# Kernel optimization log

Hardware: AMD Instinct MI355X
Metric: run time of the kernel (lower is better)

The kernel has to match this reference:

```python
import jax, jax.numpy as jnp
import numpy as np

N_NODES = 100000
D_FEAT = 128
N_EDGES = 1500000
H1 = 2 * D_FEAT  # 256, input to first linear (concat of src/dst feats)
H2 = 128


def setup_inputs() -> dict:
    key = jax.random.key(0)
    k_x, k_e, k_w1, k_w2 = jax.random.split(key, 4)
    x = jax.random.normal(k_x, (N_NODES, D_FEAT), dtype=jnp.float32)
    edge_label_index = jax.random.randint(k_e, (2, N_EDGES), 0, N_NODES, dtype=jnp.int64)
    # Kaiming-ish small init for stability
    W1 = jax.random.normal(k_w1, (H1, H2), dtype=jnp.float32) * (1.0 / np.sqrt(H1))
    b1 = jnp.zeros((H2,), dtype=jnp.float32)
    W2 = jax.random.normal(k_w2, (H2, 1), dtype=jnp.float32) * (1.0 / np.sqrt(H2))
    b2 = jnp.zeros((1,), dtype=jnp.float32)
    return {"x": x, "edge_label_index": edge_label_index,
            "W1": W1, "b1": b1, "W2": W2, "b2": b2}


def reference(x, edge_label_index, W1, b1, W2, b2):
    row, col = edge_label_index[0], edge_label_index[1]
    # gather node pair features and concat: [E, 2*D]
    h = jnp.concatenate([x[row], x[col]], axis=-1)
    h = jax.nn.relu(h @ W1 + b1)  # [E, H2]
    out = h @ W2 + b2             # [E, 1]
    return out.reshape(-1)        # [E]
```

## Files before the change

### kernel.cpp

```cpp
#include <hip/hip_runtime.h>
#include <hip/hip_bf16.h>
#include <stdint.h>

typedef __attribute__((ext_vector_type(8))) short s16x8;
typedef __attribute__((ext_vector_type(8))) unsigned short u16x8;
typedef __attribute__((ext_vector_type(4))) float f32x4;

#define D_FEAT 128
#define H2 128
#define BLOCK_THREADS 512
#define WAVES 8
#define MW 32
#define EPB (WAVES * MW)

__device__ __forceinline__ unsigned short f2bf(float f) {
  uint32_t u = __float_as_uint(f);
  return (unsigned short)((u + 0x7fffu + ((u >> 16) & 1u)) >> 16);
}

__global__ void k_cvt_x(const float* __restrict__ x, unsigned short* __restrict__ xb, int n8) {
  int i = blockIdx.x * blockDim.x + threadIdx.x;
  if (i >= n8) return;
  const f32x4* p = (const f32x4*)x + (size_t)i * 2;
  f32x4 a = p[0], b = p[1];
  u16x8 o;
  o[0] = f2bf(a[0]); o[1] = f2bf(a[1]); o[2] = f2bf(a[2]); o[3] = f2bf(a[3]);
  o[4] = f2bf(b[0]); o[5] = f2bf(b[1]); o[6] = f2bf(b[2]); o[7] = f2bf(b[3]);
  ((u16x8*)xb)[i] = o;
}

__global__ void k_cvt_w1(const float* __restrict__ W1, unsigned short* __restrict__ w1s) {
  int tid = blockIdx.x * blockDim.x + threadIdx.x;
  int lane = tid & 63;
  int kkf  = tid >> 6;
  int kk = kkf >> 3, f = kkf & 7;
  int c = lane & 15, g = lane >> 4;
  int n = f * 16 + c;
  u16x8 o;
#pragma unroll
  for (int j = 0; j < 8; ++j)
    o[j] = f2bf(W1[(kk * 32 + g * 8 + j) * H2 + n]);
  ((u16x8*)w1s)[tid] = o;
}

template <bool XBF>
__global__ __launch_bounds__(BLOCK_THREADS, 4)
void k_edge_mlp(const float* __restrict__ xf,
                const unsigned short* __restrict__ xb,
                const int* __restrict__ eli,
                const float* __restrict__ W1,
                const unsigned short* __restrict__ w1ws,
                const float* __restrict__ b1,
                const float* __restrict__ W2,
                const float* __restrict__ b2,
                float* __restrict__ out, int E, int nNodes)
{
  __shared__ alignas(16) unsigned short w1t[H2 * 256];
  const int t0   = threadIdx.x;
  const int lane = t0 & 63;
  const int wid  = t0 >> 6;
  const int c    = lane & 15;
  const int g    = lane >> 4;

  if (XBF) {
#pragma unroll
    for (int i = 0; i < 8; ++i) {
      int idx = i * BLOCK_THREADS + t0;
      ((u16x8*)w1t)[idx] = ((const u16x8*)w1ws)[idx];
    }
  } else {
#pragma unroll
    for (int i = 0; i < 8; ++i) {
      int chunk = i * BLOCK_THREADS + t0;
      int cl  = chunk & 63;
      int kkf = chunk >> 6;
      int kk = kkf >> 3, f = kkf & 7;
      int cc = cl & 15, gg = cl >> 4;
      int n = f * 16 + cc;
      u16x8 o;
#pragma unroll
      for (int j = 0; j < 8; ++j)
        o[j] = f2bf(W1[(kk * 32 + gg * 8 + j) * H2 + n]);
      ((u16x8*)w1t)[chunk] = o;
    }
  }

  const int gbase = blockIdx.x * EPB + wid * MW;
  unsigned ro[2], co[2];
#pragma unroll
  for (int m = 0; m < 2; ++m) {
    int e = gbase + m * 16 + c;
    e = e < E ? e : E - 1;
    int nr = eli[e];
    int nc = eli[E + e];
    nr = nr < 0 ? 0 : (nr >= nNodes ? nNodes - 1 : nr);
    nc = nc < 0 ? 0 : (nc >= nNodes ? nNodes - 1 : nc);
    ro[m] = (unsigned)nr * D_FEAT + g * 8;
    co[m] = (unsigned)nc * D_FEAT + g * 8;
  }

  __syncthreads();

  auto loadA = [&](int kk, s16x8* dst) {
#pragma unroll
    for (int m = 0; m < 2; ++m) {
      unsigned off = (kk < 4 ? ro[m] : co[m]) + (unsigned)((kk & 3) * 32);
      if (XBF) {
        dst[m] = *(const s16x8*)(xb + off);
      } else {
        const f32x4* q = (const f32x4*)(xf + off);
        f32x4 a = q[0], b = q[1];
        s16x8 v;
        v[0] = (short)f2bf(a[0]); v[1] = (short)f2bf(a[1]);
        v[2] = (short)f2bf(a[2]); v[3] = (short)f2bf(a[3]);
        v[4] = (short)f2bf(b[0]); v[5] = (short)f2bf(b[1]);
        v[6] = (short)f2bf(b[2]); v[7] = (short)f2bf(b[3]);
        dst[m] = v;
      }
    }
  };

  f32x4 acc[2][8];
#pragma unroll
  for (int m = 0; m < 2; ++m)
#pragma unroll
    for (int f = 0; f < 8; ++f) {
      f32x4 z = {0.f, 0.f, 0.f, 0.f};
      acc[m][f] = z;
    }

  s16x8 abuf[2][2];
  loadA(0, abuf[0]);
  loadA(1, abuf[1]);

  const unsigned short* bbase = w1t + (unsigned)lane * 8;

#pragma unroll
  for (int kk = 0; kk < 8; ++kk) {
    __builtin_amdgcn_s_setprio(1);
#pragma unroll
    for (int f = 0; f < 8; ++f) {
      s16x8 bfrag = *(const s16x8*)(bbase + (kk * 8 + f) * 512);
#pragma unroll
      for (int m = 0; m < 2; ++m)
        acc[m][f] = __builtin_amdgcn_mfma_f32_16x16x32_bf16(abuf[kk & 1][m], bfrag, acc[m][f], 0, 0, 0);
    }
    __builtin_amdgcn_s_setprio(0);
    if (kk < 6) loadA(kk + 2, abuf[kk & 1]);
  }

  float b1v[8], w2v[8];
#pragma unroll
  for (int f = 0; f < 8; ++f) {
    b1v[f] = b1[f * 16 + c];
    w2v[f] = W2[f * 16 + c];
  }
  const float b2s = b2[0];

#pragma unroll
  for (int m = 0; m < 2; ++m) {
    float sr[4];
#pragma unroll
    for (int r = 0; r < 4; ++r) {
      float s = 0.f;
#pragma unroll
      for (int f = 0; f < 8; ++f) {
        float h = acc[m][f][r] + b1v[f];
        h = h > 0.f ? h : 0.f;
        s += h * w2v[f];
      }
#pragma unroll
      for (int msk = 1; msk < 16; msk <<= 1)
        s += __shfl_xor(s, msk, 64);
      sr[r] = s;
    }
    int ebase = gbase + m * 16 + g * 4;
    if (c == 0 && ebase < E) {
      f32x4 o = {sr[0] + b2s, sr[1] + b2s, sr[2] + b2s, sr[3] + b2s};
      *(f32x4*)(out + ebase) = o;
    }
  }
}

extern "C" void kernel_launch(void* const* d_in, const int* in_sizes, int n_in,
                              void* d_out, int out_size, void* d_ws, size_t ws_size,
                              hipStream_t stream) {
  const float* x   = (const float*)d_in[0];
  const int*   eli = (const int*)d_in[1];
  const float* W1  = (const float*)d_in[2];
  const float* b1  = (const float*)d_in[3];
  const float* W2  = (const float*)d_in[4];
  const float* b2  = (const float*)d_in[5];
  float* out = (float*)d_out;

  const int E      = in_sizes[1] / 2;
  const int nNodes = in_sizes[0] / D_FEAT;

  const size_t xbytes = (size_t)nNodes * D_FEAT * 2;
  const size_t need   = xbytes + 65536;
  const bool bfpath   = (ws_size >= need);

  const int grid = (E + EPB - 1) / EPB;

  if (bfpath) {
    unsigned short* xbw  = (unsigned short*)d_ws;
    unsigned short* w1sw = (unsigned short*)((char*)d_ws + xbytes);
    int n8 = nNodes * D_FEAT / 8;
    k_cvt_x<<<(n8 + 255) / 256, 256, 0, stream>>>(x, xbw, n8);
    k_cvt_w1<<<16, 256, 0, stream>>>(W1, w1sw);
    k_edge_mlp<true><<<grid, BLOCK_THREADS, 0, stream>>>(
        x, xbw, eli, W1, w1sw, b1, W2, b2, out, E, nNodes);
  } else {
    k_edge_mlp<false><<<grid, BLOCK_THREADS, 0, stream>>>(
        x, nullptr, eli, W1, nullptr, b1, W2, b2, out, E, nNodes);
  }
}
```

Measured before the change: 137.2 us.

## Process several edge tiles per block and prefetch next tile's gathers

Each block now loops over four edge tiles instead of one, so the 64 KB W1 shared-memory staging is amortized across more work. While the epilogue (bias, ReLU, W2 dot and shuffle reduction) runs for the current tile, the next tile's indices and first A fragments are already loaded. This cuts the number of blocks by four, which reduces parallelism and may leave CUs idle at the tail.

Result: slower. 197.8 us (+44.1%).

```diff
diff --git a/kernel.cpp b/kernel.cpp
--- a/kernel.cpp
+++ b/kernel.cpp
@@ -12,6 +12,7 @@
 #define WAVES 8
 #define MW 32
 #define EPB (WAVES * MW)
+#define TPB 4
 
 __device__ __forceinline__ unsigned short f2bf(float f) {
   uint32_t u = __float_as_uint(f);
@@ -85,23 +86,26 @@
     }
   }
 
-  const int gbase = blockIdx.x * EPB + wid * MW;
-  unsigned ro[2], co[2];
-#pragma unroll
-  for (int m = 0; m < 2; ++m) {
-    int e = gbase + m * 16 + c;
-    e = e < E ? e : E - 1;
-    int nr = eli[e];
-    int nc = eli[E + e];
-    nr = nr < 0 ? 0 : (nr >= nNodes ? nNodes - 1 : nr);
-    nc = nc < 0 ? 0 : (nc >= nNodes ? nNodes - 1 : nc);
-    ro[m] = (unsigned)nr * D_FEAT + g * 8;
-    co[m] = (unsigned)nc * D_FEAT + g * 8;
-  }
-
-  __syncthreads();
-
-  auto loadA = [&](int kk, s16x8* dst) {
+  const int nt = (E + EPB - 1) / EPB;
+  int tile = blockIdx.x * TPB;
+  if (tile >= nt) return;
+  const int tend = (tile + TPB < nt) ? tile + TPB : nt;
+
+  auto mkoff = [&](int tt, unsigned* ro, unsigned* co) {
+#pragma unroll
+    for (int m = 0; m < 2; ++m) {
+      int e = tt * EPB + wid * MW + m * 16 + c;
+      e = e < E ? e : E - 1;
+      int nr = eli[e];
+      int nc = eli[E + e];
+      nr = nr < 0 ? 0 : (nr >= nNodes ? nNodes - 1 : nr);
+      nc = nc < 0 ? 0 : (nc >= nNodes ? nNodes - 1 : nc);
+      ro[m] = (unsigned)nr * D_FEAT + g * 8;
+      co[m] = (unsigned)nc * D_FEAT + g * 8;
+    }
+  };
+
+  auto loadA = [&](const unsigned* ro, const unsigned* co, int kk, s16x8* dst) {
 #pragma unroll
     for (int m = 0; m < 2; ++m) {
       unsigned off = (kk < 4 ? ro[m] : co[m]) + (unsigned)((kk & 3) * 32);
@@ -120,65 +124,92 @@
     }
   };
 
-  f32x4 acc[2][8];
-#pragma unroll
-  for (int m = 0; m < 2; ++m)
+  __syncthreads();
+
+  const unsigned short* bbase = w1t + (unsigned)lane * 8;
+
+  unsigned ro[2], co[2];
+  mkoff(tile, ro, co);
+  s16x8 abuf[2][2];
+  loadA(ro, co, 0, abuf[0]);
+  loadA(ro, co, 1, abuf[1]);
+
+  const float b2s = b2[0];
+
+  while (true) {
+    f32x4 acc[2][8];
+#pragma unroll
+    for (int m = 0; m < 2; ++m)
+#pragma unroll
+      for (int f = 0; f < 8; ++f) {
+        f32x4 z = {0.f, 0.f, 0.f, 0.f};
+        acc[m][f] = z;
+      }
+
+#pragma unroll
+    for (int kk = 0; kk < 8; ++kk) {
+      __builtin_amdgcn_s_setprio(1);
+#pragma unroll
+      for (int f = 0; f < 8; ++f) {
+        s16x8 bfrag = *(const s16x8*)(bbase + (kk * 8 + f) * 512);
+#pragma unroll
+        for (int m = 0; m < 2; ++m)
+          acc[m][f] = __builtin_amdgcn_mfma_f32_16x16x32_bf16(abuf[kk & 1][m], bfrag, acc[m][f], 0, 0, 0);
+      }
+      __builtin_amdgcn_s_setprio(0);
+      if (kk < 6) loadA(ro, co, kk + 2, abuf[kk & 1]);
+    }
+
+    float b1v[8], w2v[8];
 #pragma unroll
     for (int f = 0; f < 8; ++f) {
-      f32x4 z = {0.f, 0.f, 0.f, 0.f};
-      acc[m][f] = z;
-    }
-
-  s16x8 abuf[2][2];
-  loadA(0, abuf[0]);
-  loadA(1, abuf[1]);
-
-  const unsigned short* bbase = w1t + (unsigned)lane * 8;
-
-#pragma unroll
-  for (int kk = 0; kk < 8; ++kk) {
-    __builtin_amdgcn_s_setprio(1);
-#pragma unroll
-    for (int f = 0; f < 8; ++f) {
-      s16x8 bfrag = *(const s16x8*)(bbase + (kk * 8 + f) * 512);
-#pragma unroll
-      for (int m = 0; m < 2; ++m)
-        acc[m][f] = __builtin_amdgcn_mfma_f32_16x16x32_bf16(abuf[kk & 1][m], bfrag, acc[m][f], 0, 0, 0);
-    }
-    __builtin_amdgcn_s_setprio(0);
-    if (kk < 6) loadA(kk + 2, abuf[kk & 1]);
-  }
-
-  float b1v[8], w2v[8];
-#pragma unroll
-  for (int f = 0; f < 8; ++f) {
-    b1v[f] = b1[f * 16 + c];
-    w2v[f] = W2[f * 16 + c];
-  }
-  const float b2s = b2[0];
-
-#pragma unroll
-  for (int m = 0; m < 2; ++m) {
-    float sr[4];
-#pragma unroll
-    for (int r = 0; r < 4; ++r) {
-      float s = 0.f;
-#pragma unroll
-      for (int f = 0; f < 8; ++f) {
-        float h = acc[m][f][r] + b1v[f];
-        h = h > 0.f ? h : 0.f;
-        s += h * w2v[f];
-      }
-#pragma unroll
-      for (int msk = 1; msk < 16; msk <<= 1)
-        s += __shfl_xor(s, msk, 64);
-      sr[r] = s;
-    }
-    int ebase = gbase + m * 16 + g * 4;
-    if (c == 0 && ebase < E) {
-      f32x4 o = {sr[0] + b2s, sr[1] + b2s, sr[2] + b2s, sr[3] + b2s};
-      *(f32x4*)(out + ebase) = o;
-    }
+      b1v[f] = b1[f * 16 + c];
+      w2v[f] = W2[f * 16 + c];
+    }
+    float pre[2][4];
+#pragma unroll
+    for (int m = 0; m < 2; ++m)
+#pragma unroll
+      for (int r = 0; r < 4; ++r) {
+        float s = 0.f;
+#pragma unroll
+        for (int f = 0; f < 8; ++f) {
+          float h = acc[m][f][r] + b1v[f];
+          h = h > 0.f ? h : 0.f;
+          s += h * w2v[f];
+        }
+        pre[m][r] = s;
+      }
+
+    const int gbase = tile * EPB + wid * MW;
+    const bool more = (tile + 1 < tend);
+
+    if (more) {
+      mkoff(tile + 1, ro, co);
+      loadA(ro, co, 0, abuf[0]);
+      loadA(ro, co, 1, abuf[1]);
+    }
+
+#pragma unroll
+    for (int m = 0; m < 2; ++m) {
+      float sr[4];
+#pragma unroll
+      for (int r = 0; r < 4; ++r) {
+        float s = pre[m][r];
+#pragma unroll
+        for (int msk = 1; msk < 16; msk <<= 1)
+          s += __shfl_xor(s, msk, 64);
+        sr[r] = s;
+      }
+      int ebase = gbase + m * 16 + g * 4;
+      if (c == 0 && ebase < E) {
+        f32x4 o = {sr[0] + b2s, sr[1] + b2s, sr[2] + b2s, sr[3] + b2s};
+        *(f32x4*)(out + ebase) = o;
+      }
+    }
+
+    if (!more) break;
+    ++tile;
   }
 }
 
@@ -200,7 +231,8 @@
   const size_t need   = xbytes + 65536;
   const bool bfpath   = (ws_size >= need);
 
-  const int grid = (E + EPB - 1) / EPB;
+  const int nt   = (E + EPB - 1) / EPB;
+  const int grid = (nt + TPB - 1) / TPB;
 
   if (bfpath) {
     unsigned short* xbw  = (unsigned short*)d_ws;
```

## Precompute per-node W1 projections and reduce edge MLP to gather-add-dot

Applied to the files above, without the earlier changes.

Uses linearity of the first layer to split [x_r, x_c] @ W1 into per-node projections u = x@W1_top + b1 and v = x@W1_bot, computed once per node with MFMA and stored as bf16. The edge kernel then only gathers u[row] and v[col], applies ReLU to the sum and takes the dot product with W2. This removes the per-edge matmul, which is about 15x more work than the per-node one, at the cost of an extra pass writing two node-sized tables. It also adds a second bf16 rounding of the intermediate projections.

After: 148.2 us. +8.0%, slower.

```diff
diff --git a/kernel.cpp b/kernel.cpp
--- a/kernel.cpp
+++ b/kernel.cpp
@@ -8,25 +8,13 @@
 
 #define D_FEAT 128
 #define H2 128
-#define BLOCK_THREADS 512
-#define WAVES 8
-#define MW 32
-#define EPB (WAVES * MW)
 
 __device__ __forceinline__ unsigned short f2bf(float f) {
   uint32_t u = __float_as_uint(f);
   return (unsigned short)((u + 0x7fffu + ((u >> 16) & 1u)) >> 16);
 }
-
-__global__ void k_cvt_x(const float* __restrict__ x, unsigned short* __restrict__ xb, int n8) {
-  int i = blockIdx.x * blockDim.x + threadIdx.x;
-  if (i >= n8) return;
-  const f32x4* p = (const f32x4*)x + (size_t)i * 2;
-  f32x4 a = p[0], b = p[1];
-  u16x8 o;
-  o[0] = f2bf(a[0]); o[1] = f2bf(a[1]); o[2] = f2bf(a[2]); o[3] = f2bf(a[3]);
-  o[4] = f2bf(b[0]); o[5] = f2bf(b[1]); o[6] = f2bf(b[2]); o[7] = f2bf(b[3]);
-  ((u16x8*)xb)[i] = o;
+__device__ __forceinline__ float bf2f(unsigned short s) {
+  return __uint_as_float((uint32_t)s << 16);
 }
 
 __global__ void k_cvt_w1(const float* __restrict__ W1, unsigned short* __restrict__ w1s) {
@@ -43,80 +31,217 @@
   ((u16x8*)w1s)[tid] = o;
 }
 
-template <bool XBF>
-__global__ __launch_bounds__(BLOCK_THREADS, 4)
-void k_edge_mlp(const float* __restrict__ xf,
-                const unsigned short* __restrict__ xb,
+__global__ void k_cvt_w2p(const float* __restrict__ W2, float* __restrict__ w2p) {
+  int s = threadIdx.x;
+  w2p[s] = W2[(s & 7) * 16 + (s >> 3)];
+}
+
+__global__ __launch_bounds__(256, 4)
+void k_uv(const float* __restrict__ x,
+          const unsigned short* __restrict__ w1ws,
+          const float* __restrict__ b1,
+          unsigned short* __restrict__ u,
+          unsigned short* __restrict__ v,
+          int nNodes)
+{
+  __shared__ alignas(16) unsigned short w1t[H2 * 256];
+  const int t0 = threadIdx.x, lane = t0 & 63, wid = t0 >> 6;
+  const int c = lane & 15, g = lane >> 4;
+
+#pragma unroll
+  for (int i = 0; i < 16; ++i) {
+    int idx = i * 256 + t0;
+    ((u16x8*)w1t)[idx] = ((const u16x8*)w1ws)[idx];
+  }
+
+  const int nb = blockIdx.x * 128 + wid * 32;
+  s16x8 af[4][2];
+#pragma unroll
+  for (int m = 0; m < 2; ++m) {
+    int node = nb + m * 16 + c;
+    node = node < nNodes ? node : nNodes - 1;
+    const float* xp = x + (size_t)node * D_FEAT;
+#pragma unroll
+    for (int kk = 0; kk < 4; ++kk) {
+      const f32x4* q = (const f32x4*)(xp + kk * 32 + g * 8);
+      f32x4 a = q[0], b = q[1];
+      s16x8 vv;
+      vv[0] = (short)f2bf(a[0]); vv[1] = (short)f2bf(a[1]);
+      vv[2] = (short)f2bf(a[2]); vv[3] = (short)f2bf(a[3]);
+      vv[4] = (short)f2bf(b[0]); vv[5] = (short)f2bf(b[1]);
+      vv[6] = (short)f2bf(b[2]); vv[7] = (short)f2bf(b[3]);
+      af[kk][m] = vv;
+    }
+  }
+  float b1v[8];
+#pragma unroll
+  for (int f = 0; f < 8; ++f) b1v[f] = b1[f * 16 + c];
+
+  __syncthreads();
+  const unsigned short* bbase = w1t + (unsigned)lane * 8;
+
+  f32x4 acc[2][8];
+
+#pragma unroll
+  for (int m = 0; m < 2; ++m)
+#pragma unroll
+    for (int f = 0; f < 8; ++f) {
+      f32x4 z = {b1v[f], b1v[f], b1v[f], b1v[f]};
+      acc[m][f] = z;
+    }
+#pragma unroll
+  for (int kk = 0; kk < 4; ++kk)
+#pragma unroll
+    for (int f = 0; f < 8; ++f) {
+      s16x8 bfrag = *(const s16x8*)(bbase + (kk * 8 + f) * 512);
+#pragma unroll
+      for (int m = 0; m < 2; ++m)
+        acc[m][f] = __builtin_amdgcn_mfma_f32_16x16x32_bf16(af[kk][m], bfrag, acc[m][f], 0, 0, 0);
+    }
+#pragma unroll
+  for (int m = 0; m < 2; ++m)
+#pragma unroll
+    for (int r = 0; r < 4; ++r) {
+      int node = nb + m * 16 + g * 4 + r;
+      if (node < nNodes) {
+        u16x8 o;
+#pragma unroll
+        for (int f = 0; f < 8; ++f) o[f] = f2bf(acc[m][f][r]);
+        *(u16x8*)(u + (size_t)node * H2 + c * 8) = o;
+      }
+    }
+
+#pragma unroll
+  for (int m = 0; m < 2; ++m)
+#pragma unroll
+    for (int f = 0; f < 8; ++f) {
+      f32x4 z = {0.f, 0.f, 0.f, 0.f};
+      acc[m][f] = z;
+    }
+#pragma unroll
+  for (int kk = 0; kk < 4; ++kk)
+#pragma unroll
+    for (int f = 0; f < 8; ++f) {
+      s16x8 bfrag = *(const s16x8*)(bbase + ((kk + 4) * 8 + f) * 512);
+#pragma unroll
+      for (int m = 0; m < 2; ++m)
+        acc[m][f] = __builtin_amdgcn_mfma_f32_16x16x32_bf16(af[kk][m], bfrag, acc[m][f], 0, 0, 0);
+    }
+#pragma unroll
+  for (int m = 0; m < 2; ++m)
+#pragma unroll
+    for (int r = 0; r < 4; ++r) {
+      int node = nb + m * 16 + g * 4 + r;
+      if (node < nNodes) {
+        u16x8 o;
+#pragma unroll
+        for (int f = 0; f < 8; ++f) o[f] = f2bf(acc[m][f][r]);
+        *(u16x8*)(v + (size_t)node * H2 + c * 8) = o;
+      }
+    }
+}
+
+__global__ __launch_bounds__(256, 8)
+void k_edge(const unsigned short* __restrict__ u,
+            const unsigned short* __restrict__ v,
+            const int* __restrict__ eli,
+            const float* __restrict__ w2p,
+            const float* __restrict__ b2,
+            float* __restrict__ out, int E, int nNodes)
+{
+  const int t0 = threadIdx.x, lane = t0 & 63, wid = t0 >> 6;
+  const int c = lane & 15, g = lane >> 4;
+  const int ebase = blockIdx.x * 64 + wid * 16;
+
+  int e = ebase + c;
+  e = e < E ? e : E - 1;
+  int nr = eli[e], nc = eli[E + e];
+  nr = nr < 0 ? 0 : (nr >= nNodes ? nNodes - 1 : nr);
+  nc = nc < 0 ? 0 : (nc >= nNodes ? nNodes - 1 : nc);
+  const unsigned short* up = u + (size_t)nr * H2 + g * 8;
+  const unsigned short* vp = v + (size_t)nc * H2 + g * 8;
+
+  u16x8 uu[4], vv[4];
+#pragma unroll
+  for (int kk = 0; kk < 4; ++kk) {
+    uu[kk] = *(const u16x8*)(up + kk * 32);
+    vv[kk] = *(const u16x8*)(vp + kk * 32);
+  }
+
+  float s = 0.f;
+#pragma unroll
+  for (int kk = 0; kk < 4; ++kk) {
+    const f32x4* wq = (const f32x4*)(w2p + kk * 32 + g * 8);
+    f32x4 w0 = wq[0], w1 = wq[1];
+#pragma unroll
+    for (int j = 0; j < 8; ++j) {
+      float h = bf2f(uu[kk][j]) + bf2f(vv[kk][j]);
+      h = h > 0.f ? h : 0.f;
+      float w = (j < 4) ? w0[j & 3] : w1[j & 3];
+      s += h * w;
+    }
+  }
+  s += __shfl_xor(s, 16, 64);
+  s += __shfl_xor(s, 32, 64);
+  if (g == 0) {
+    int eo = ebase + c;
+    if (eo < E) out[eo] = s + b2[0];
+  }
+}
+
+__global__ __launch_bounds__(512, 4)
+void k_fallback(const float* __restrict__ xf,
                 const int* __restrict__ eli,
                 const float* __restrict__ W1,
-                const unsigned short* __restrict__ w1ws,
                 const float* __restrict__ b1,
                 const float* __restrict__ W2,
                 const float* __restrict__ b2,
                 float* __restrict__ out, int E, int nNodes)
 {
   __shared__ alignas(16) unsigned short w1t[H2 * 256];
-  const int t0   = threadIdx.x;
-  const int lane = t0 & 63;
-  const int wid  = t0 >> 6;
-  const int c    = lane & 15;
-  const int g    = lane >> 4;
-
-  if (XBF) {
-#pragma unroll
-    for (int i = 0; i < 8; ++i) {
-      int idx = i * BLOCK_THREADS + t0;
-      ((u16x8*)w1t)[idx] = ((const u16x8*)w1ws)[idx];
-    }
-  } else {
-#pragma unroll
-    for (int i = 0; i < 8; ++i) {
-      int chunk = i * BLOCK_THREADS + t0;
-      int cl  = chunk & 63;
-      int kkf = chunk >> 6;
-      int kk = kkf >> 3, f = kkf & 7;
-      int cc = cl & 15, gg = cl >> 4;
-      int n = f * 16 + cc;
-      u16x8 o;
-#pragma unroll
-      for (int j = 0; j < 8; ++j)
-        o[j] = f2bf(W1[(kk * 32 + gg * 8 + j) * H2 + n]);
-      ((u16x8*)w1t)[chunk] = o;
-    }
-  }
-
-  const int gbase = blockIdx.x * EPB + wid * MW;
+  const int t0 = threadIdx.x, lane = t0 & 63, wid = t0 >> 6;
+  const int c = lane & 15, g = lane >> 4;
+
+#pragma unroll
+  for (int i = 0; i < 8; ++i) {
+    int chunk = i * 512 + t0;
+    int cl = chunk & 63, kkf = chunk >> 6;
+    int kk = kkf >> 3, f = kkf & 7;
+    int cc = cl & 15, gg = cl >> 4;
+    int n = f * 16 + cc;
+    u16x8 o;
+#pragma unroll
+    for (int j = 0; j < 8; ++j)
+      o[j] = f2bf(W1[(kk * 32 + gg * 8 + j) * H2 + n]);
+    ((u16x8*)w1t)[chunk] = o;
+  }
+
+  const int gbase = blockIdx.x * 256 + wid * 32;
   unsigned ro[2], co[2];
 #pragma unroll
   for (int m = 0; m < 2; ++m) {
     int e = gbase + m * 16 + c;
     e = e < E ? e : E - 1;
-    int nr = eli[e];
-    int nc = eli[E + e];
+    int nr = eli[e], nc = eli[E + e];
     nr = nr < 0 ? 0 : (nr >= nNodes ? nNodes - 1 : nr);
     nc = nc < 0 ? 0 : (nc >= nNodes ? nNodes - 1 : nc);
     ro[m] = (unsigned)nr * D_FEAT + g * 8;
     co[m] = (unsigned)nc * D_FEAT + g * 8;
   }
-
   __syncthreads();
 
   auto loadA = [&](int kk, s16x8* dst) {
 #pragma unroll
     for (int m = 0; m < 2; ++m) {
       unsigned off = (kk < 4 ? ro[m] : co[m]) + (unsigned)((kk & 3) * 32);
-      if (XBF) {
-        dst[m] = *(const s16x8*)(xb + off);
-      } else {
-        const f32x4* q = (const f32x4*)(xf + off);
-        f32x4 a = q[0], b = q[1];
-        s16x8 v;
-        v[0] = (short)f2bf(a[0]); v[1] = (short)f2bf(a[1]);
-        v[2] = (short)f2bf(a[2]); v[3] = (short)f2bf(a[3]);
-        v[4] = (short)f2bf(b[0]); v[5] = (short)f2bf(b[1]);
-        v[6] = (short)f2bf(b[2]); v[7] = (short)f2bf(b[3]);
-        dst[m] = v;
-      }
+      const f32x4* q = (const f32x4*)(xf + off);
+      f32x4 a = q[0], b = q[1];
+      s16x8 vv2;
+      vv2[0] = (short)f2bf(a[0]); vv2[1] = (short)f2bf(a[1]);
+      vv2[2] = (short)f2bf(a[2]); vv2[3] = (short)f2bf(a[3]);
+      vv2[4] = (short)f2bf(b[0]); vv2[5] = (short)f2bf(b[1]);
+      vv2[6] = (short)f2bf(b[2]); vv2[7] = (short)f2bf(b[3]);
+      dst[m] = vv2;
     }
   };
 
@@ -128,16 +253,12 @@
       f32x4 z = {0.f, 0.f, 0.f, 0.f};
       acc[m][f] = z;
     }
-
   s16x8 abuf[2][2];
   loadA(0, abuf[0]);
   loadA(1, abuf[1]);
-
   const unsigned short* bbase = w1t + (unsigned)lane * 8;
-
 #pragma unroll
   for (int kk = 0; kk < 8; ++kk) {
-    __builtin_amdgcn_s_setprio(1);
 #pragma unroll
     for (int f = 0; f < 8; ++f) {
       s16x8 bfrag = *(const s16x8*)(bbase + (kk * 8 + f) * 512);
@@ -145,18 +266,12 @@
       for (int m = 0; m < 2; ++m)
         acc[m][f] = __builtin_amdgcn_mfma_f32_16x16x32_bf16(abuf[kk & 1][m], bfrag, acc[m][f], 0, 0, 0);
     }
-    __builtin_amdgcn_s_setprio(0);
     if (kk < 6) loadA(kk + 2, abuf[kk & 1]);
   }
-
   float b1v[8], w2v[8];
 #pragma unroll
-  for (int f = 0; f < 8; ++f) {
-    b1v[f] = b1[f * 16 + c];
-    w2v[f] = W2[f * 16 + c];
-  }
+  for (int f = 0; f < 8; ++f) { b1v[f] = b1[f * 16 + c]; w2v[f] = W2[f * 16 + c]; }
   const float b2s = b2[0];
-
 #pragma unroll
   for (int m = 0; m < 2; ++m) {
     float sr[4];
@@ -170,14 +285,13 @@
         s += h * w2v[f];
       }
 #pragma unroll
-      for (int msk = 1; msk < 16; msk <<= 1)
-        s += __shfl_xor(s, msk, 64);
+      for (int msk = 1; msk < 16; msk <<= 1) s += __shfl_xor(s, msk, 64);
       sr[r] = s;
     }
-    int ebase = gbase + m * 16 + g * 4;
-    if (c == 0 && ebase < E) {
+    int ebase2 = gbase + m * 16 + g * 4;
+    if (c == 0 && ebase2 < E) {
       f32x4 o = {sr[0] + b2s, sr[1] + b2s, sr[2] + b2s, sr[3] + b2s};
-      *(f32x4*)(out + ebase) = o;
+      *(f32x4*)(out + ebase2) = o;
     }
   }
 }
@@ -196,22 +310,20 @@
   const int E      = in_sizes[1] / 2;
   const int nNodes = in_sizes[0] / D_FEAT;
 
-  const size_t xbytes = (size_t)nNodes * D_FEAT * 2;
-  const size_t need   = xbytes + 65536;
-  const bool bfpath   = (ws_size >= need);
-
-  const int grid = (E + EPB - 1) / EPB;
-
-  if (bfpath) {
-    unsigned short* xbw  = (unsigned short*)d_ws;
-    unsigned short* w1sw = (unsigned short*)((char*)d_ws + xbytes);
-    int n8 = nNodes * D_FEAT / 8;
-    k_cvt_x<<<(n8 + 255) / 256, 256, 0, stream>>>(x, xbw, n8);
-    k_cvt_w1<<<16, 256, 0, stream>>>(W1, w1sw);
-    k_edge_mlp<true><<<grid, BLOCK_THREADS, 0, stream>>>(
-        x, xbw, eli, W1, w1sw, b1, W2, b2, out, E, nNodes);
+  const size_t ubytes = (size_t)nNodes * H2 * 2;
+  const size_t need   = 2 * ubytes + 65536 + 512;
+
+  if (ws_size >= need) {
+    unsigned short* us  = (unsigned short*)d_ws;
+    unsigned short* vs  = (unsigned short*)((char*)d_ws + ubytes);
+    unsigned short* w1f = (unsigned short*)((char*)d_ws + 2 * ubytes);
+    float*          w2p = (float*)((char*)d_ws + 2 * ubytes + 65536);
+
+    k_cvt_w1<<<16, 256, 0, stream>>>(W1, w1f);
+    k_cvt_w2p<<<1, 128, 0, stream>>>(W2, w2p);
+    k_uv<<<(nNodes + 127) / 128, 256, 0, stream>>>(x, w1f, b1, us, vs, nNodes);
+    k_edge<<<(E + 63) / 64, 256, 0, stream>>>(us, vs, eli, w2p, b2, out, E, nNodes);
   } else {
-    k_edge_mlp<false><<<grid, BLOCK_THREADS, 0, stream>>>(
-        x, nullptr, eli, W1, nullptr, b1, W2, b2, out, E, nNodes);
-  }
-}
+    k_fallback<<<(E + 255) / 256, 512, 0, stream>>>(x, eli, W1, b1, W2, b2, out, E, nNodes);
+  }
+}
```
